# Performance work log

Measured on AMD Instinct MI355X. Metric: run time of the kernel, lower is better.

Reference implementation:

```python
import math
import jax, jax.numpy as jnp
import numpy as np

L, H, D, FF, V, S = 12, 12, 768, 3072, 32000, 1024
HD = D // H
EPS = 1e-5
B, T = 2, 1024


def layernorm(x, w, b):
    mu = jnp.mean(x, axis=-1, keepdims=True)
    var = jnp.mean(jnp.square(x - mu), axis=-1, keepdims=True)
    return (x - mu) * jax.lax.rsqrt(var + EPS) * w + b


def setup_inputs() -> dict:
    key = jax.random.key(0)
    ks = jax.random.split(key, 12)
    std = 0.02
    std_res = 0.02 / math.sqrt(2 * L)  # out_proj / down_proj scaled init
    return {
        "input_ids": jax.random.randint(ks[0], (B, T), 0, V),
        "tok_emb": jax.random.normal(ks[1], (V, D), jnp.float32) * std,
        "pos_emb": jax.random.normal(ks[2], (S, D), jnp.float32) * std,
        "ln1_w": jnp.ones((L, D), jnp.float32),
        "ln1_b": jnp.zeros((L, D), jnp.float32),
        "qkv_w": jax.random.normal(ks[3], (L, 3 * D, D), jnp.float32) * std,
        "out_w": jax.random.normal(ks[4], (L, D, D), jnp.float32) * std_res,
        "ln2_w": jnp.ones((L, D), jnp.float32),
        "ln2_b": jnp.zeros((L, D), jnp.float32),
        "up_w": jax.random.normal(ks[5], (L, FF, D), jnp.float32) * std,
        "down_w": jax.random.normal(ks[6], (L, D, FF), jnp.float32) * std_res,
        "lnf_w": jnp.ones((D,), jnp.float32),
        "lnf_b": jnp.zeros((D,), jnp.float32),
    }


def reference(input_ids, tok_emb, pos_emb, ln1_w, ln1_b, qkv_w, out_w,
              ln2_w, ln2_b, up_w, down_w, lnf_w, lnf_b):
    b, t = input_ids.shape
    x = tok_emb[input_ids] + pos_emb[:t]  # (B,T,D); dropout = eval no-op
    causal = jnp.tril(jnp.ones((t, t), bool))  # (T,T)
    scale = 1.0 / math.sqrt(HD)

    def block(x, p):
        l1w, l1b, qkvw, ow, l2w, l2b, uw, dw = p
        h = layernorm(x, l1w, l1b)
        qkv = h @ qkvw.T  # (B,T,3D)
        q, k, v = jnp.split(qkv, 3, axis=-1)
        q = q.reshape(b, t, H, HD)
        k = k.reshape(b, t, H, HD)
        v = v.reshape(b, t, H, HD)
        scores = jnp.einsum('bihd,bjhd->bhij', q, k) * scale
        scores = jnp.where(causal, scores, -jnp.inf)
        probs = jax.nn.softmax(scores, axis=-1)  # attn_dropout = eval no-op
        o = jnp.einsum('bhij,bjhd->bihd', probs, v).reshape(b, t, D)
        x = x + o @ ow.T
        h2 = layernorm(x, l2w, l2b)
        x = x + jax.nn.gelu(h2 @ uw.T, approximate=False) @ dw.T
        return x, None

    x, _ = jax.lax.scan(block, x, (ln1_w, ln1_b, qkv_w, out_w, ln2_w, ln2_b, up_w, down_w))
    x = layernorm(x, lnf_w, lnf_b)
    logits = x @ tok_emb.T  # tied lm_head
    return logits
```

## Files before the change

kernel.cpp:

```cpp
#include <hip/hip_runtime.h>
#include <hip/hip_bf16.h>
#include <math.h>

#define L_  12
#define H_  12
#define D_  768
#define FF_ 3072
#define V_  32000
#define T_  1024
#define B_  2
#define BT_ (B_*T_)

typedef unsigned short ushort_t;
typedef unsigned int   uint_t;
typedef __bf16 bf16x8 __attribute__((ext_vector_type(8)));
typedef float  f32x4  __attribute__((ext_vector_type(4)));

__device__ __forceinline__ uint_t f2bf1(float f) {
    uint_t u = __builtin_bit_cast(uint_t, f);
    return (u + 0x7FFFu + ((u >> 16) & 1u)) >> 16;
}
__device__ __forceinline__ uint_t f2bf2(float lo, float hi) {
    return f2bf1(lo) | (f2bf1(hi) << 16);
}
__device__ __forceinline__ float bf2f(ushort_t u) {
    return __builtin_bit_cast(float, (uint_t)u << 16);
}

__device__ __forceinline__ void gl_lds16(const ushort_t* g, ushort_t* l) {
    __builtin_amdgcn_global_load_lds(
        (const __attribute__((address_space(1))) uint_t*)g,
        (__attribute__((address_space(3))) uint_t*)l, 16, 0, 0);
}

__global__ __launch_bounds__(256) void cast_bf16(const float* __restrict__ in,
                                                 ushort_t* __restrict__ out, int n8)
{
    for (int i = blockIdx.x * 256 + threadIdx.x; i < n8; i += gridDim.x * 256) {
        const float4* p = (const float4*)(in + (size_t)i * 8);
        float4 a = p[0], b = p[1];
        *(uint4*)(out + (size_t)i * 8) =
            make_uint4(f2bf2(a.x,a.y), f2bf2(a.z,a.w), f2bf2(b.x,b.y), f2bf2(b.z,b.w));
    }
}

__device__ __forceinline__ void cast_body(const float* __restrict__ q,
    const float* __restrict__ o, const float* __restrict__ u, const float* __restrict__ d,
    ushort_t* __restrict__ out, int bid, int nb)
{
    const int N0 = 3*D_*D_/8, N1 = N0 + D_*D_/8, N2 = N1 + FF_*D_/8, N3 = N2 + D_*FF_/8;
    for (int i = bid * 256 + threadIdx.x; i < N3; i += nb * 256) {
        const float* src;
        if      (i < N0) src = q + (size_t)i * 8;
        else if (i < N1) src = o + (size_t)(i - N0) * 8;
        else if (i < N2) src = u + (size_t)(i - N1) * 8;
        else             src = d + (size_t)(i - N2) * 8;
        const float4* p = (const float4*)src;
        float4 a = p[0], b = p[1];
        *(uint4*)(out + (size_t)i * 8) =
            make_uint4(f2bf2(a.x,a.y), f2bf2(a.z,a.w), f2bf2(b.x,b.y), f2bf2(b.z,b.w));
    }
}

#define EPI_F32   0
#define EPI_BF16  1
#define EPI_GELU  2
#define EPI_PART  3
#define EPI_QKV   4

template <int EPI, int BM, int KS>
__global__ __launch_bounds__(256) void gemm_bt(
    const ushort_t* __restrict__ A, const ushort_t* __restrict__ W,
    void* Cv, ushort_t* __restrict__ Vt, int N, int K, int Kc)
{
    constexpr int MI = BM / 32;
    constexpr int AH = BM * 64;
    constexpr int BH = 128 * 64;
    __shared__ ushort_t As[2 * AH];
    __shared__ ushort_t Bs[2 * BH];

    const int tid  = threadIdx.x;
    const int w    = tid >> 6;
    const int lane = tid & 63;

    const int nwg = gridDim.x;
    int swz = (blockIdx.x & 7) * (nwg >> 3) + (blockIdx.x >> 3);
    constexpr int MT = 2048 / BM;
    const int mt = swz & (MT - 1);
    int rest     = swz / MT;
    const int ks = rest & (KS - 1);
    const int nt = rest / KS;
    const int m0 = mt * BM, n0 = nt * 128;
    const int kb = ks * Kc;

    const int srow = lane >> 3;
    const int scol = ((lane & 7) ^ srow) * 8;
    const ushort_t* gA = A + (size_t)(m0 + w * (BM / 4) + srow) * K + scol;
    const ushort_t* gW = W + (size_t)(n0 + w * 32 + srow) * K + scol;
    const size_t row8 = (size_t)8 * K;

    const int lr = lane & 15;
    const int lg = lane >> 4;
    const int wm = (w >> 1) * (BM / 2);
    const int wn = (w & 1) * 64;

    f32x4 acc[MI][4] = {};

    auto stage = [&](int buf, int k0) {
        ushort_t* lA = As + buf * AH + w * (BM / 4) * 64;
        ushort_t* lB = Bs + buf * BH + w * 2048;
        #pragma unroll
        for (int i = 0; i < BM / 32; ++i)
            gl_lds16(gA + k0 + i * row8, lA + i * 512);
        #pragma unroll
        for (int i = 0; i < 4; ++i)
            gl_lds16(gW + k0 + i * row8, lB + i * 512);
    };

    stage(0, kb);
    __syncthreads();
    int cur = 0;
    for (int k0 = kb; k0 < kb + Kc; k0 += 64) {
        if (k0 + 64 < kb + Kc) stage(cur ^ 1, k0 + 64);
        const ushort_t* Ab = As + cur * AH;
        const ushort_t* Bb = Bs + cur * BH;
        __builtin_amdgcn_s_setprio(1);
        #pragma unroll
        for (int kk = 0; kk < 2; ++kk) {
            bf16x8 av[MI], bv[4];
            #pragma unroll
            for (int i = 0; i < MI; ++i) {
                int rr = wm + i * 16 + lr;
                int ch = (lg + 4 * kk) ^ (rr & 7);
                av[i] = *(const bf16x8*)&Ab[rr * 64 + ch * 8];
            }
            #pragma unroll
            for (int j = 0; j < 4; ++j) {
                int rr = wn + j * 16 + lr;
                int ch = (lg + 4 * kk) ^ (rr & 7);
                bv[j] = *(const bf16x8*)&Bb[rr * 64 + ch * 8];
            }
            #pragma unroll
            for (int i = 0; i < MI; ++i)
                #pragma unroll
                for (int j = 0; j < 4; ++j)
                    acc[i][j] = __builtin_amdgcn_mfma_f32_16x16x32_bf16(av[i], bv[j], acc[i][j], 0, 0, 0);
        }
        __builtin_amdgcn_s_setprio(0);
        __syncthreads();
        cur ^= 1;
    }

    float*    Cf = (float*)Cv;
    ushort_t* Cb = (ushort_t*)Cv;
    ushort_t* Pp = (EPI == EPI_PART) ? ((ushort_t*)Cv + (size_t)ks * BT_ * D_) : nullptr;
    const int rbase = lg * 4;
    #pragma unroll
    for (int i = 0; i < MI; ++i) {
        #pragma unroll
        for (int j = 0; j < 4; ++j) {
            const int row0 = m0 + wm + i * 16 + rbase;
            const int col  = n0 + wn + j * 16 + lr;
            if (EPI == EPI_QKV) {
                if (col < 1536) {
                    #pragma unroll
                    for (int r = 0; r < 4; ++r)
                        Cb[(size_t)(row0 + r) * 2304 + col] = (ushort_t)f2bf1(acc[i][j][r]);
                } else {
                    const int hh = (col - 1536) >> 6, dd = (col - 1536) & 63;
                    const int bb = row0 >> 10,        tt = row0 & 1023;
                    uint2 pk;
                    pk.x = f2bf2(acc[i][j][0], acc[i][j][1]);
                    pk.y = f2bf2(acc[i][j][2], acc[i][j][3]);
                    *(uint2*)&Vt[(((size_t)bb * H_ + hh) * 64 + dd) * T_ + tt] = pk;
                }
            } else {
                #pragma unroll
                for (int r = 0; r < 4; ++r) {
                    size_t idx = (size_t)(row0 + r) * N + col;
                    float v = acc[i][j][r];
                    if (EPI == EPI_F32)  Cf[idx] = v;
                    if (EPI == EPI_BF16) Cb[idx] = (ushort_t)f2bf1(v);
                    if (EPI == EPI_GELU) Cb[idx] = (ushort_t)f2bf1(0.5f * v * (1.0f + erff(v * 0.70710678118654752f)));
                    if (EPI == EPI_PART) Pp[idx] = (ushort_t)f2bf1(v);
                }
            }
        }
    }
}

__global__ __launch_bounds__(512, 2) void gemm256(
    const ushort_t* __restrict__ A, const ushort_t* __restrict__ W,
    float* __restrict__ C, int N, int K)
{
    __shared__ ushort_t Ls[2][2][256 * 64];

    const int tid  = threadIdx.x;
    const int w    = tid >> 6;
    const int lane = tid & 63;

    const int nwg = gridDim.x;
    int swz = (blockIdx.x & 7) * (nwg >> 3) + (blockIdx.x >> 3);
    const int mt = swz & 7;
    const int nt = swz >> 3;
    const int m0 = mt * 256, n0 = nt * 256;

    const int trow = tid >> 3;
    const int tchk = (tid & 7) ^ (trow & 7);
    const ushort_t* gA = A + (size_t)(m0 + trow) * K + tchk * 8;
    const ushort_t* gW = W + (size_t)(n0 + trow) * K + tchk * 8;

    const int lr = lane & 15;
    const int lg = lane >> 4;
    const int wm = (w >> 2) * 128;
    const int wn = (w & 3) * 64;

    f32x4 acc[8][4] = {};

    auto stage = [&](int buf, int k0) {
        #pragma unroll
        for (int seg = 0; seg < 4; ++seg) {
            gl_lds16(gA + (size_t)(seg * 64) * K + k0, &Ls[buf][0][seg * 4096 + w * 512]);
            gl_lds16(gW + (size_t)(seg * 64) * K + k0, &Ls[buf][1][seg * 4096 + w * 512]);
        }
    };

    stage(0, 0);
    __syncthreads();
    int cur = 0;
    const int NT = K / 64;
    for (int t = 0; t < NT; ++t) {
        if (t + 1 < NT) stage(cur ^ 1, (t + 1) * 64);
        const ushort_t* Ab = Ls[cur][0];
        const ushort_t* Bb = Ls[cur][1];
        bf16x8 bv[4][2];
        #pragma unroll
        for (int nf = 0; nf < 4; ++nf) {
            int rr = wn + nf * 16 + lr;
            #pragma unroll
            for (int kk = 0; kk < 2; ++kk) {
                int ch = (kk * 4 + lg) ^ (rr & 7);
                bv[nf][kk] = *(const bf16x8*)&Bb[rr * 64 + ch * 8];
            }
        }
        __builtin_amdgcn_s_setprio(1);
        #pragma unroll
        for (int mf = 0; mf < 8; ++mf) {
            int rr = wm + mf * 16 + lr;
            int ch0 = lg ^ (rr & 7);
            int ch1 = (4 + lg) ^ (rr & 7);
            bf16x8 a0 = *(const bf16x8*)&Ab[rr * 64 + ch0 * 8];
            bf16x8 a1 = *(const bf16x8*)&Ab[rr * 64 + ch1 * 8];
            #pragma unroll
            for (int nf = 0; nf < 4; ++nf) {
                acc[mf][nf] = __builtin_amdgcn_mfma_f32_16x16x32_bf16(a0, bv[nf][0], acc[mf][nf], 0, 0, 0);
                acc[mf][nf] = __builtin_amdgcn_mfma_f32_16x16x32_bf16(a1, bv[nf][1], acc[mf][nf], 0, 0, 0);
            }
        }
        __builtin_amdgcn_s_setprio(0);
        __syncthreads();
        cur ^= 1;
    }

    const int rbase = lg * 4;
    #pragma unroll
    for (int mf = 0; mf < 8; ++mf) {
        #pragma unroll
        for (int nf = 0; nf < 4; ++nf) {
            #pragma unroll
            for (int r = 0; r < 4; ++r) {
                int row = m0 + wm + mf * 16 + rbase + r;
                int col = n0 + wn + nf * 16 + lr;
                C[(size_t)row * N + col] = acc[mf][nf][r];
            }
        }
    }
}

__global__ __launch_bounds__(64) void attn_mfma(const ushort_t* __restrict__ qkv,
    const ushort_t* __restrict__ vt, ushort_t* __restrict__ o)
{
    __shared__ ushort_t Ps[16 * 136];

    int swz = (blockIdx.x & 7) * 192 + (blockIdx.x >> 3);
    const int bh  = swz >> 6;
    const int qtl = 63 - (swz & 63);
    const int b   = bh / H_;
    const int h   = bh % H_;
    const int lane = threadIdx.x;
    const int l15  = lane & 15;
    const int lg   = lane >> 4;
    const int qbase = qtl * 16;
    const int qlast = qbase + 15;

    const ushort_t* qp = qkv + ((size_t)(b * T_) + qbase + l15) * 2304 + h * 64 + lg * 8;
    bf16x8 qf0 = *(const bf16x8*)qp;
    bf16x8 qf1 = *(const bf16x8*)(qp + 32);

    f32x4 od[4] = {};
    float mr[4] = {-INFINITY, -INFINITY, -INFINITY, -INFINITY};
    float lr[4] = {0.f, 0.f, 0.f, 0.f};

    const ushort_t* kbase = qkv + (size_t)(b * T_) * 2304 + 768 + h * 64;
    const ushort_t* vbase = vt + (size_t)bh * 64 * T_;
    const float SC = 0.18033688011112042f;

    for (int j0 = 0; j0 <= qlast; j0 += 128) {
        f32x4 s[8];
        __builtin_amdgcn_s_setprio(1);
        #pragma unroll
        for (int n = 0; n < 8; ++n) {
            if (j0 + 16 * n <= qlast) {
                const ushort_t* kr = kbase + (size_t)(j0 + 16 * n + l15) * 2304 + lg * 8;
                bf16x8 kf0 = *(const bf16x8*)kr;
                bf16x8 kf1 = *(const bf16x8*)(kr + 32);
                f32x4 a = {};
                a = __builtin_amdgcn_mfma_f32_16x16x32_bf16(qf0, kf0, a, 0, 0, 0);
                a = __builtin_amdgcn_mfma_f32_16x16x32_bf16(qf1, kf1, a, 0, 0, 0);
                s[n] = a;
            } else {
                s[n] = f32x4{-INFINITY, -INFINITY, -INFINITY, -INFINITY};
            }
        }
        __builtin_amdgcn_s_setprio(0);

        #pragma unroll
        for (int n = 0; n < 8; ++n) {
            #pragma unroll
            for (int r = 0; r < 4; ++r) {
                float v = s[n][r] * SC;
                int jg = j0 + 16 * n + l15;
                int qg = qbase + lg * 4 + r;
                if (jg > qg) v = -INFINITY;
                s[n][r] = v;
            }
        }

        float al[4];
        #pragma unroll
        for (int r = 0; r < 4; ++r) {
            float tm = fmaxf(fmaxf(fmaxf(s[0][r], s[1][r]), fmaxf(s[2][r], s[3][r])),
                             fmaxf(fmaxf(s[4][r], s[5][r]), fmaxf(s[6][r], s[7][r])));
            tm = fmaxf(tm, __shfl_xor(tm, 1, 64));
            tm = fmaxf(tm, __shfl_xor(tm, 2, 64));
            tm = fmaxf(tm, __shfl_xor(tm, 4, 64));
            tm = fmaxf(tm, __shfl_xor(tm, 8, 64));
            float mn = fmaxf(mr[r], tm);
            al[r] = exp2f(mr[r] - mn);
            mr[r] = mn;
        }
        #pragma unroll
        for (int n = 0; n < 8; ++n)
            #pragma unroll
            for (int r = 0; r < 4; ++r)
                s[n][r] = exp2f(s[n][r] - mr[r]);
        #pragma unroll
        for (int r = 0; r < 4; ++r) {
            float ps = (s[0][r] + s[1][r]) + (s[2][r] + s[3][r]);
            ps += (s[4][r] + s[5][r]) + (s[6][r] + s[7][r]);
            ps += __shfl_xor(ps, 1, 64);
            ps += __shfl_xor(ps, 2, 64);
            ps += __shfl_xor(ps, 4, 64);
            ps += __shfl_xor(ps, 8, 64);
            lr[r] = lr[r] * al[r] + ps;
        }
        #pragma unroll
        for (int n = 0; n < 4; ++n)
            #pragma unroll
            for (int r = 0; r < 4; ++r)
                od[n][r] *= al[r];

        #pragma unroll
        for (int n = 0; n < 8; ++n)
            #pragma unroll
            for (int r = 0; r < 4; ++r)
                Ps[(lg * 4 + r) * 136 + 16 * n + l15] = (ushort_t)f2bf1(s[n][r]);

        __builtin_amdgcn_s_setprio(1);
        #pragma unroll
        for (int kc = 0; kc < 4; ++kc) {
            if (j0 + kc * 32 <= qlast) {
                bf16x8 pa = *(const bf16x8*)&Ps[l15 * 136 + kc * 32 + lg * 8];
                #pragma unroll
                for (int nn = 0; nn < 4; ++nn) {
                    bf16x8 vf = *(const bf16x8*)&vbase[(size_t)(16 * nn + l15) * T_ + j0 + kc * 32 + lg * 8];
                    od[nn] = __builtin_amdgcn_mfma_f32_16x16x32_bf16(pa, vf, od[nn], 0, 0, 0);
                }
            }
        }
        __builtin_amdgcn_s_setprio(0);
    }

    #pragma unroll
    for (int r = 0; r < 4; ++r) {
        float inv = 1.0f / lr[r];
        int row = qbase + lg * 4 + r;
        ushort_t* op = o + ((size_t)(b * T_ + row)) * 768 + h * 64 + l15;
        #pragma unroll
        for (int nn = 0; nn < 4; ++nn)
            op[16 * nn] = (ushort_t)f2bf1(od[nn][r] * inv);
    }
}

__device__ __forceinline__ void ln_body(float v0, float v1, float v2,
    const float* __restrict__ w, const float* __restrict__ bia,
    ushort_t* __restrict__ orow, int tid)
{
    float s  = v0 + v1 + v2;
    float s2 = v0 * v0 + v1 * v1 + v2 * v2;
    #pragma unroll
    for (int off = 32; off > 0; off >>= 1) {
        s  += __shfl_down(s,  off, 64);
        s2 += __shfl_down(s2, off, 64);
    }
    __shared__ float sh[8];
    const int wave = tid >> 6;
    if ((tid & 63) == 0) { sh[wave] = s; sh[4 + wave] = s2; }
    __syncthreads();
    float S  = sh[0] + sh[1] + sh[2] + sh[3];
    float S2 = sh[4] + sh[5] + sh[6] + sh[7];
    float mean = S * (1.f / 768.f);
    float var  = S2 * (1.f / 768.f) - mean * mean;
    float inv  = rsqrtf(var + 1e-5f);
    orow[tid]       = (ushort_t)f2bf1((v0 - mean) * inv * w[tid]       + bia[tid]);
    orow[tid + 256] = (ushort_t)f2bf1((v1 - mean) * inv * w[tid + 256] + bia[tid + 256]);
    orow[tid + 512] = (ushort_t)f2bf1((v2 - mean) * inv * w[tid + 512] + bia[tid + 512]);
}

__device__ __forceinline__ void ln_red4_body(float* __restrict__ x,
    const ushort_t* __restrict__ P, const float* __restrict__ w,
    const float* __restrict__ bia, ushort_t* __restrict__ out, int row)
{
    const int tid = threadIdx.x;
    const size_t base = (size_t)row * 768;
    const size_t st = (size_t)BT_ * D_;
    float v0 = x[base + tid];
    float v1 = x[base + tid + 256];
    float v2 = x[base + tid + 512];
    #pragma unroll
    for (int p = 0; p < 4; ++p) {
        v0 += bf2f(P[p * st + base + tid]);
        v1 += bf2f(P[p * st + base + tid + 256]);
        v2 += bf2f(P[p * st + base + tid + 512]);
    }
    x[base + tid]       = v0;
    x[base + tid + 256] = v1;
    x[base + tid + 512] = v2;
    ln_body(v0, v1, v2, w, bia, out + base, tid);
}

__global__ __launch_bounds__(256) void ln_red4_cast(float* __restrict__ x,
    const ushort_t* __restrict__ P, const float* __restrict__ w,
    const float* __restrict__ bia, ushort_t* __restrict__ out,
    const float* __restrict__ cq, const float* __restrict__ co,
    const float* __restrict__ cu, const float* __restrict__ cd,
    ushort_t* __restrict__ wout)
{
    if (blockIdx.x < 2048)
        ln_red4_body(x, P, w, bia, out, blockIdx.x);
    else
        cast_body(cq, co, cu, cd, wout, blockIdx.x - 2048, 1024);
}

__global__ __launch_bounds__(256) void ln_red4(float* __restrict__ x,
    const ushort_t* __restrict__ P, const float* __restrict__ w,
    const float* __restrict__ bia, ushort_t* __restrict__ out)
{
    ln_red4_body(x, P, w, bia, out, blockIdx.x);
}

__global__ __launch_bounds__(256) void embed_ln_cast(const int* __restrict__ ids,
    const float* __restrict__ tok, const float* __restrict__ pos,
    const float* __restrict__ w, const float* __restrict__ bia,
    float* __restrict__ x, ushort_t* __restrict__ out,
    const float* __restrict__ cq, const float* __restrict__ co,
    const float* __restrict__ cu, const float* __restrict__ cd,
    ushort_t* __restrict__ wout)
{
    if (blockIdx.x < 2048) {
        const int bt = blockIdx.x;
        const int t  = bt % T_;
        const int id = ids[bt];
        const int tid = threadIdx.x;
        const float* tr = tok + (size_t)id * 768;
        const float* pr = pos + (size_t)t * 768;
        const size_t base = (size_t)bt * 768;
        float v0 = tr[tid]       + pr[tid];
        float v1 = tr[tid + 256] + pr[tid + 256];
        float v2 = tr[tid + 512] + pr[tid + 512];
        x[base + tid]       = v0;
        x[base + tid + 256] = v1;
        x[base + tid + 512] = v2;
        ln_body(v0, v1, v2, w, bia, out + base, tid);
    } else {
        cast_body(cq, co, cu, cd, wout, blockIdx.x - 2048, 1024);
    }
}

extern "C" void kernel_launch(void* const* d_in, const int* in_sizes, int n_in,
                              void* d_out, int out_size, void* d_ws, size_t ws_size,
                              hipStream_t stream)
{
    const int*   ids   = (const int*)  d_in[0];
    const float* tok   = (const float*)d_in[1];
    const float* pos   = (const float*)d_in[2];
    const float* ln1w  = (const float*)d_in[3];
    const float* ln1b  = (const float*)d_in[4];
    const float* qkvw  = (const float*)d_in[5];
    const float* outw  = (const float*)d_in[6];
    const float* ln2w  = (const float*)d_in[7];
    const float* ln2b  = (const float*)d_in[8];
    const float* upw   = (const float*)d_in[9];
    const float* downw = (const float*)d_in[10];
    const float* lnfw  = (const float*)d_in[11];
    const float* lnfb  = (const float*)d_in[12];
    float* out = (float*)d_out;

    char* ws = (char*)d_ws;
    ushort_t* h    = (ushort_t*)ws;
    float*    x    = (float*)   (ws + 3145728);
    ushort_t* qkv  = (ushort_t*)(ws + 9437184);
    ushort_t* o    = qkv  + (size_t)BT_ * 3 * D_;
    ushort_t* vt   = o    + (size_t)BT_ * D_;
    ushort_t* ffh  = vt   + (size_t)B_ * H_ * 64 * T_;
    ushort_t* P4   = (ushort_t*)(ws + 37748736);
    ushort_t* layerW = (ushort_t*)(ws + 50331648);
    ushort_t* tokW   = (ushort_t*)(ws + 67108864);

    ushort_t* qkvwB  = layerW;
    ushort_t* outwB  = qkvwB + (size_t)3 * D_ * D_;
    ushort_t* upwB   = outwB + (size_t)D_ * D_;
    ushort_t* downwB = upwB  + (size_t)FF_ * D_;

    for (int l = 0; l < L_; ++l) {
        const float* cq = qkvw  + (size_t)l * 3 * D_ * D_;
        const float* co = outw  + (size_t)l * D_ * D_;
        const float* cu = upw   + (size_t)l * FF_ * D_;
        const float* cd = downw + (size_t)l * D_ * FF_;

        if (l == 0)
            embed_ln_cast<<<3072, 256, 0, stream>>>(ids, tok, pos, ln1w, ln1b, x, h,
                                                    cq, co, cu, cd, layerW);
        else
            ln_red4_cast<<<3072, 256, 0, stream>>>(x, P4, ln1w + l * D_, ln1b + l * D_, h,
                                                   cq, co, cu, cd, layerW);

        gemm_bt<EPI_QKV, 64, 1><<<32 * (3 * D_ / 128), 256, 0, stream>>>(
            h, qkvwB, qkv, vt, 3 * D_, D_, D_);

        attn_mfma<<<B_ * H_ * (T_ / 16), 64, 0, stream>>>(qkv, vt, o);

        gemm_bt<EPI_PART, 64, 4><<<32 * (D_ / 128) * 4, 256, 0, stream>>>(
            o, outwB, P4, nullptr, D_, D_, D_ / 4);

        ln_red4<<<BT_, 256, 0, stream>>>(x, P4, ln2w + l * D_, ln2b + l * D_, h);

        gemm_bt<EPI_GELU, 64, 1><<<32 * (FF_ / 128), 256, 0, stream>>>(
            h, upwB, ffh, nullptr, FF_, D_, D_);

        gemm_bt<EPI_PART, 64, 4><<<32 * (D_ / 128) * 4, 256, 0, stream>>>(
            ffh, downwB, P4, nullptr, D_, FF_, FF_ / 4);
    }

    ln_red4<<<BT_, 256, 0, stream>>>(x, P4, lnfw, lnfb, h);

    cast_bf16<<<2048, 256, 0, stream>>>(tok, tokW, V_ * D_ / 8);
    gemm256<<<(2048 / 256) * (V_ / 256), 512, 0, stream>>>(h, tokW, out, V_, D_);
}
```

Measured before the change: 1.821 ms.

## Triple-buffer LM-head GEMM with BK=32 and fuse final LN with tok cast

```diff
diff --git a/kernel.cpp b/kernel.cpp
--- a/kernel.cpp
+++ b/kernel.cpp
@@ -33,10 +33,10 @@
         (__attribute__((address_space(3))) uint_t*)l, 16, 0, 0);
 }
 
-__global__ __launch_bounds__(256) void cast_bf16(const float* __restrict__ in,
-                                                 ushort_t* __restrict__ out, int n8)
-{
-    for (int i = blockIdx.x * 256 + threadIdx.x; i < n8; i += gridDim.x * 256) {
+__device__ __forceinline__ void castN_body(const float* __restrict__ in,
+    ushort_t* __restrict__ out, int n8, int bid, int nb)
+{
+    for (int i = bid * 256 + threadIdx.x; i < n8; i += nb * 256) {
         const float4* p = (const float4*)(in + (size_t)i * 8);
         float4 a = p[0], b = p[1];
         *(uint4*)(out + (size_t)i * 8) =
@@ -193,7 +193,7 @@
     const ushort_t* __restrict__ A, const ushort_t* __restrict__ W,
     float* __restrict__ C, int N, int K)
 {
-    __shared__ ushort_t Ls[2][2][256 * 64];
+    __shared__ ushort_t Ls[3][2][256 * 32];
 
     const int tid  = threadIdx.x;
     const int w    = tid >> 6;
@@ -205,10 +205,11 @@
     const int nt = swz >> 3;
     const int m0 = mt * 256, n0 = nt * 256;
 
-    const int trow = tid >> 3;
-    const int tchk = (tid & 7) ^ (trow & 7);
-    const ushort_t* gA = A + (size_t)(m0 + trow) * K + tchk * 8;
-    const ushort_t* gW = W + (size_t)(n0 + trow) * K + tchk * 8;
+    const int srow = tid >> 2;
+    const int schk = ((tid & 3) ^ ((srow >> 1) & 3)) * 8;
+    const ushort_t* gA = A + (size_t)(m0 + srow) * K + schk;
+    const ushort_t* gW = W + (size_t)(n0 + srow) * K + schk;
+    const size_t row128 = (size_t)128 * K;
 
     const int lr = lane & 15;
     const int lg = lane >> 4;
@@ -218,48 +219,44 @@
     f32x4 acc[8][4] = {};
 
     auto stage = [&](int buf, int k0) {
-        #pragma unroll
-        for (int seg = 0; seg < 4; ++seg) {
-            gl_lds16(gA + (size_t)(seg * 64) * K + k0, &Ls[buf][0][seg * 4096 + w * 512]);
-            gl_lds16(gW + (size_t)(seg * 64) * K + k0, &Ls[buf][1][seg * 4096 + w * 512]);
-        }
+        gl_lds16(gA + k0,          &Ls[buf][0][w * 512]);
+        gl_lds16(gA + k0 + row128, &Ls[buf][0][4096 + w * 512]);
+        gl_lds16(gW + k0,          &Ls[buf][1][w * 512]);
+        gl_lds16(gW + k0 + row128, &Ls[buf][1][4096 + w * 512]);
     };
 
+    const int NT = K / 32;
     stage(0, 0);
-    __syncthreads();
-    int cur = 0;
-    const int NT = K / 64;
+    stage(1, 32);
+    int cb = 0, nb_ = 1, pb = 2;
     for (int t = 0; t < NT; ++t) {
-        if (t + 1 < NT) stage(cur ^ 1, (t + 1) * 64);
-        const ushort_t* Ab = Ls[cur][0];
-        const ushort_t* Bb = Ls[cur][1];
-        bf16x8 bv[4][2];
+        if (t == NT - 1) asm volatile("s_waitcnt vmcnt(0)" ::: "memory");
+        else             asm volatile("s_waitcnt vmcnt(4)" ::: "memory");
+        __builtin_amdgcn_s_barrier();
+
+        const ushort_t* Ab = Ls[cb][0];
+        const ushort_t* Bb = Ls[cb][1];
+        bf16x8 bv[4];
         #pragma unroll
         for (int nf = 0; nf < 4; ++nf) {
             int rr = wn + nf * 16 + lr;
-            #pragma unroll
-            for (int kk = 0; kk < 2; ++kk) {
-                int ch = (kk * 4 + lg) ^ (rr & 7);
-                bv[nf][kk] = *(const bf16x8*)&Bb[rr * 64 + ch * 8];
-            }
+            int ch = lg ^ ((rr >> 1) & 3);
+            bv[nf] = *(const bf16x8*)&Bb[rr * 32 + ch * 8];
         }
         __builtin_amdgcn_s_setprio(1);
         #pragma unroll
         for (int mf = 0; mf < 8; ++mf) {
             int rr = wm + mf * 16 + lr;
-            int ch0 = lg ^ (rr & 7);
-            int ch1 = (4 + lg) ^ (rr & 7);
-            bf16x8 a0 = *(const bf16x8*)&Ab[rr * 64 + ch0 * 8];
-            bf16x8 a1 = *(const bf16x8*)&Ab[rr * 64 + ch1 * 8];
-            #pragma unroll
-            for (int nf = 0; nf < 4; ++nf) {
-                acc[mf][nf] = __builtin_amdgcn_mfma_f32_16x16x32_bf16(a0, bv[nf][0], acc[mf][nf], 0, 0, 0);
-                acc[mf][nf] = __builtin_amdgcn_mfma_f32_16x16x32_bf16(a1, bv[nf][1], acc[mf][nf], 0, 0, 0);
-            }
+            int ch = lg ^ ((rr >> 1) & 3);
+            bf16x8 a0 = *(const bf16x8*)&Ab[rr * 32 + ch * 8];
+            #pragma unroll
+            for (int nf = 0; nf < 4; ++nf)
+                acc[mf][nf] = __builtin_amdgcn_mfma_f32_16x16x32_bf16(a0, bv[nf], acc[mf][nf], 0, 0, 0);
         }
         __builtin_amdgcn_s_setprio(0);
-        __syncthreads();
-        cur ^= 1;
+
+        if (t + 2 < NT) stage(pb, (t + 2) * 32);
+        int tmp = cb; cb = nb_; nb_ = pb; pb = tmp;
     }
 
     const int rbase = lg * 4;
@@ -467,6 +464,17 @@
     const float* __restrict__ bia, ushort_t* __restrict__ out)
 {
     ln_red4_body(x, P, w, bia, out, blockIdx.x);
+}
+
+__global__ __launch_bounds__(256) void ln_red4_tok(float* __restrict__ x,
+    const ushort_t* __restrict__ P, const float* __restrict__ w,
+    const float* __restrict__ bia, ushort_t* __restrict__ out,
+    const float* __restrict__ tok, ushort_t* __restrict__ tokW)
+{
+    if (blockIdx.x < 2048)
+        ln_red4_body(x, P, w, bia, out, blockIdx.x);
+    else
+        castN_body(tok, tokW, V_ * D_ / 8, blockIdx.x - 2048, 2048);
 }
 
 __global__ __launch_bounds__(256) void embed_ln_cast(const int* __restrict__ ids,
@@ -562,8 +570,6 @@
             ffh, downwB, P4, nullptr, D_, FF_, FF_ / 4);
     }
 
-    ln_red4<<<BT_, 256, 0, stream>>>(x, P4, lnfw, lnfb, h);
-
-    cast_bf16<<<2048, 256, 0, stream>>>(tok, tokW, V_ * D_ / 8);
+    ln_red4_tok<<<4096, 256, 0, stream>>>(x, P4, lnfw, lnfb, h, tok, tokW);
     gemm256<<<(2048 / 256) * (V_ / 256), 512, 0, stream>>>(h, tokW, out, V_, D_);
 }
```

Measured after the change: 1.832 ms. No clear change (+0.6%).
